# Optimization experiments

Hardware: AMD Instinct MI355X
Metric: run time of the kernel (lower is better)

The kernel has to match this reference:

```python
import jax, jax.numpy as jnp
import numpy as np

B, S, NX, H = 8, 1024, 1024, 16
HD = NX // H  # head dim = 64
MASKED_BIAS = -10000.0


def setup_inputs() -> dict:
    key = jax.random.key(0)
    ks = jax.random.split(key, 6)
    return {
        "x": jax.random.normal(ks[0], (B, S, NX), dtype=jnp.float32),
        "query": jax.random.normal(ks[1], (B, S, NX), dtype=jnp.float32),
        "c_attn_w": jax.random.normal(ks[2], (NX, 3 * NX), dtype=jnp.float32) * 0.02,
        "c_attn_b": jnp.zeros((3 * NX,), dtype=jnp.float32),
        "c_proj_w": jax.random.normal(ks[3], (NX, NX), dtype=jnp.float32) * 0.02,
        "c_proj_b": jnp.zeros((NX,), dtype=jnp.float32),
    }


def _split_heads(t):
    # [B, S, NX] -> [B, H, S, HD]
    b, s, _ = t.shape
    return t.reshape(b, s, H, HD).transpose(0, 2, 1, 3)


def reference(x, query, c_attn_w, c_attn_b, c_proj_w, c_proj_b):
    # Conv1D: y = x @ W + b
    kv = x @ c_attn_w + c_attn_b          # [B,S,3NX]; use key/value slices
    qy = query @ c_attn_w + c_attn_b      # [B,S,3NX]; use query slice
    q = _split_heads(qy[..., :NX])                     # [B,H,S,HD]
    k = _split_heads(kv[..., NX:2 * NX])               # [B,H,S,HD]
    v = _split_heads(kv[..., 2 * NX:])                 # [B,H,S,HD]

    w = jnp.einsum("bhqd,bhkd->bhqk", q, k) / jnp.sqrt(jnp.float32(HD))
    causal = jnp.tril(jnp.ones((S, S), dtype=bool))[None, None]
    w = jnp.where(causal, w, jnp.float32(MASKED_BIAS))
    w = jax.nn.softmax(w, axis=-1)
    a = jnp.einsum("bhqk,bhkd->bhqd", w, v)            # [B,H,S,HD]
    a = a.transpose(0, 2, 1, 3).reshape(B, S, NX)      # merge heads
    return a @ c_proj_w + c_proj_b
```

## Files before the change

### kernel.cpp

```cpp
#include <hip/hip_runtime.h>
#include <cstdint>
#include <cstddef>

#define Bb   8
#define Ss   1024
#define NXx  1024
#define Hh   16
#define HDd  64
#define Mm   (Bb*Ss)

typedef __bf16 bf16x8 __attribute__((ext_vector_type(8)));
typedef float  f32x4  __attribute__((ext_vector_type(4)));

__device__ __forceinline__ unsigned short f2bf(float f) {
    union { float f; unsigned int u; } v; v.f = f;
    return (unsigned short)((v.u + 0x8000u) >> 16);
}

__device__ __forceinline__ void load_lds16(const unsigned short* g, unsigned short* lds_base) {
    __builtin_amdgcn_global_load_lds(
        (const __attribute__((address_space(1))) void*)g,
        (__attribute__((address_space(3))) void*)lds_base, 16, 0, 0);
}

__global__ __launch_bounds__(256) void prep(
    const float* __restrict__ x, const float* __restrict__ query,
    const float* __restrict__ caw, const float* __restrict__ cpw,
    unsigned short* __restrict__ xb, unsigned short* __restrict__ qb,
    unsigned short* __restrict__ Wt, unsigned short* __restrict__ Pt)
{
    __shared__ float tile[32][33];
    const int bid = blockIdx.x;
    const int tid = threadIdx.x;

    if (bid < 16384) {
        const float* in = (bid < 8192) ? x : query;
        unsigned short* out = (bid < 8192) ? xb : qb;
        const int i = ((bid & 8191) * 256 + tid) * 4;
        const float4 v = *(const float4*)(in + i);
        unsigned long long p = (unsigned long long)f2bf(v.x)
            | ((unsigned long long)f2bf(v.y) << 16)
            | ((unsigned long long)f2bf(v.z) << 32)
            | ((unsigned long long)f2bf(v.w) << 48);
        *(unsigned long long*)(out + i) = p;
        return;
    }

    const float* in;
    unsigned short* out;
    int C, t;
    if (bid < 16384 + 3072) { in = caw; out = Wt; C = 3072; t = bid - 16384; }
    else                    { in = cpw; out = Pt; C = 1024; t = bid - 19456; }
    const int ntx = C >> 5;
    const int c0 = (t % ntx) * 32, r0 = (t / ntx) * 32;
    const int tx = tid & 31, ty = tid >> 5;
    for (int i = ty; i < 32; i += 8)
        tile[i][tx] = in[(size_t)(r0 + i) * C + c0 + tx];
    __syncthreads();
    for (int i = ty; i < 32; i += 8)
        out[(size_t)(c0 + i) * 1024 + r0 + tx] = f2bf(tile[tx][i]);
}

__global__ __launch_bounds__(256) void gemm128(
    const unsigned short* __restrict__ Ax,
    const unsigned short* __restrict__ Aq,
    const unsigned short* __restrict__ Bt,
    const float* __restrict__ bias,
    int K, int mode,
    unsigned short* __restrict__ out_q,
    unsigned short* __restrict__ out_k,
    unsigned short* __restrict__ out_v,
    float* __restrict__ out_f)
{
    __shared__ unsigned short smem[16384];
    unsigned short (*As)[64] = (unsigned short (*)[64])(smem);
    unsigned short (*Bs)[64] = (unsigned short (*)[64])(smem + 8192);

    const int tid  = threadIdx.x;
    const int w    = tid >> 6;
    const int lane = tid & 63;

    const int nx   = (mode == 0) ? 24 : 8;
    const int nxh  = nx >> 1;
    const int n    = blockIdx.x;
    const int xcd  = n & 7;
    const int sgrp = n >> 3;
    const int m0   = ((xcd >> 1) * 16 + sgrp / nxh) * 128;
    const int n0   = ((xcd & 1) * nxh + sgrp % nxh) * 128;
    const int region = n0 >> 10;
    const unsigned short* A = (mode == 0 && region == 0) ? Aq : Ax;

    const int wm   = (w >> 1) * 64;
    const int wn   = (w & 1) * 64;
    const int lrow = lane & 15;
    const int quad = lane >> 4;

    f32x4 acc[4][4] = {};

    const int rr   = lane >> 3;
    const int scol = (((lane & 7) ^ ((lane >> 4) & 3)) << 3);
    const unsigned short* Ag = A  + (size_t)(m0 + w * 32 + rr) * K + scol;
    const unsigned short* Bg = Bt + (size_t)(n0 + w * 32 + rr) * K + scol;
    unsigned short* ldsA = smem + (w * 32) * 64;
    unsigned short* ldsB = smem + 8192 + (w * 32) * 64;

    const int sw = (lrow >> 1) & 3;

    for (int k0 = 0; k0 < K; k0 += 64) {
        __syncthreads();
#pragma unroll
        for (int c = 0; c < 4; ++c) {
            load_lds16(Ag + (size_t)(c * 8) * K + k0, ldsA + c * 512);
            load_lds16(Bg + (size_t)(c * 8) * K + k0, ldsB + c * 512);
        }
        __syncthreads();
#pragma unroll
        for (int kk = 0; kk < 2; ++kk) {
            bf16x8 af[4], bfr[4];
            const int pc = (((kk * 4 + quad) ^ sw) << 3);
#pragma unroll
            for (int i = 0; i < 4; ++i) {
                af[i]  = *(const bf16x8*)&As[wm + i * 16 + lrow][pc];
                bfr[i] = *(const bf16x8*)&Bs[wn + i * 16 + lrow][pc];
            }
#pragma unroll
            for (int i = 0; i < 4; ++i)
#pragma unroll
                for (int j = 0; j < 4; ++j)
                    acc[i][j] = __builtin_amdgcn_mfma_f32_16x16x32_bf16(af[i], bfr[j], acc[i][j], 0, 0, 0);
        }
    }

    __syncthreads();

    if (mode == 1) {
#pragma unroll
        for (int i = 0; i < 4; ++i)
#pragma unroll
            for (int j = 0; j < 4; ++j) {
                const int ncol = n0 + wn + j * 16 + lrow;
                const float bv = bias[ncol];
#pragma unroll
                for (int r = 0; r < 4; ++r) {
                    const int mrow = m0 + wm + i * 16 + quad * 4 + r;
                    out_f[(size_t)mrow * NXx + ncol] = acc[i][j][r] + bv;
                }
            }
        return;
    }

    unsigned short* ep = smem + w * 2048;

    if (region != 2) {
        unsigned short* outp = (region == 0) ? out_q : out_k;
#pragma unroll
        for (int j = 0; j < 4; ++j) {
            const float bv = bias[n0 + wn + j * 16 + lrow];
#pragma unroll
            for (int i = 0; i < 4; ++i)
#pragma unroll
                for (int r = 0; r < 4; ++r)
                    ep[(i * 16 + quad * 4 + r) * 24 + lrow] = f2bf(acc[i][j][r] + bv);
#pragma unroll
            for (int t = 0; t < 2; ++t) {
                const int c    = t * 64 + lane;
                const int row  = c >> 1, ch = (c & 1) * 8;
                const int mrow = m0 + wm + row;
                const int cc   = (n0 + wn + j * 16 + ch) & (NXx - 1);
                const int hh   = cc >> 6, dd = cc & 63;
                const int bh   = (mrow >> 10) * Hh + hh;
                const int ss   = mrow & (Ss - 1);
                *(uint4*)&outp[((size_t)bh * Ss + ss) * HDd + dd] =
                    *(const uint4*)&ep[row * 24 + ch];
            }
        }
    } else {
#pragma unroll
        for (int j = 0; j < 4; ++j) {
            const float bv = bias[n0 + wn + j * 16 + lrow];
#pragma unroll
            for (int i = 0; i < 4; ++i)
#pragma unroll
                for (int r = 0; r < 4; ++r)
                    ep[lrow * 72 + i * 16 + quad * 4 + r] = f2bf(acc[i][j][r] + bv);
#pragma unroll
            for (int t = 0; t < 2; ++t) {
                const int c    = t * 64 + lane;
                const int col  = c >> 3, rc = (c & 7) * 8;
                const int cc   = (n0 + wn + j * 16 + col) & (NXx - 1);
                const int hh   = cc >> 6, dd = cc & 63;
                const int mrow = m0 + wm + rc;
                const int bh   = (mrow >> 10) * Hh + hh;
                const int ss   = mrow & (Ss - 1);
                *(uint4*)&out_v[((size_t)bh * HDd + dd) * Ss + ss] =
                    *(const uint4*)&ep[col * 72 + rc];
            }
        }
    }
}

__global__ __launch_bounds__(256) void flash_attn(
    const unsigned short* __restrict__ Qh,
    const unsigned short* __restrict__ Kh,
    const unsigned short* __restrict__ Vt,
    unsigned short* __restrict__ about)
{
    __shared__ unsigned short Ks[64][64];
    __shared__ unsigned short Vs[64][64];
    __shared__ unsigned short Pl[4][16][72];

    const int tid  = threadIdx.x;
    const int w    = tid >> 6;
    const int lane = tid & 63;
    const int bh   = blockIdx.x & 127;
    const int pr   = blockIdx.x >> 7;
    const int b    = bh >> 4, h = bh & 15;
    const int lrow = lane & 15;
    const int quad = lane >> 4;

    const unsigned short* Qb = Qh + (size_t)bh * Ss * HDd;
    const unsigned short* Kb = Kh + (size_t)bh * Ss * HDd;
    const unsigned short* Vb = Vt + (size_t)bh * HDd * Ss;

    const int sr = lane >> 3;
    const int lc = (((lane & 7) ^ ((lane >> 4) & 3)) << 3);
    unsigned short* ldsK0 = &Ks[w * 16][0];
    unsigned short* ldsK1 = &Ks[w * 16 + 8][0];
    unsigned short* ldsV0 = &Vs[w * 16][0];
    unsigned short* ldsV1 = &Vs[w * 16 + 8][0];

    const int sw = (lrow >> 1) & 3;
    const int ca = ((quad ^ sw) << 3);
    const int cb = (((4 + quad) ^ sw) << 3);

    for (int half = 0; half < 2; ++half) {
        const int qt    = half ? (15 - pr) : pr;
        const int qBase = qt * 64 + w * 16;

        const bf16x8 aq0 = *(const bf16x8*)(Qb + (size_t)(qBase + lrow) * HDd + quad * 8);
        const bf16x8 aq1 = *(const bf16x8*)(Qb + (size_t)(qBase + lrow) * HDd + 32 + quad * 8);

        f32x4 O[4] = {};
        float lsum[4] = { 0.f, 0.f, 0.f, 0.f };

        const int nkt = qt + 1;
        for (int kt = 0; kt < nkt; ++kt) {
            const int k0 = kt * 64;

            __syncthreads();
            load_lds16(Kb + (size_t)(k0 + w * 16 + sr) * HDd + lc,     ldsK0);
            load_lds16(Kb + (size_t)(k0 + w * 16 + sr + 8) * HDd + lc, ldsK1);
            load_lds16(Vb + (size_t)(w * 16 + sr) * Ss + k0 + lc,      ldsV0);
            load_lds16(Vb + (size_t)(w * 16 + sr + 8) * Ss + k0 + lc,  ldsV1);
            __syncthreads();

            f32x4 s[4] = {};
#pragma unroll
            for (int j = 0; j < 4; ++j) {
                bf16x8 b0 = *(const bf16x8*)&Ks[j * 16 + lrow][ca];
                bf16x8 b1 = *(const bf16x8*)&Ks[j * 16 + lrow][cb];
                s[j] = __builtin_amdgcn_mfma_f32_16x16x32_bf16(aq0, b0, s[j], 0, 0, 0);
                s[j] = __builtin_amdgcn_mfma_f32_16x16x32_bf16(aq1, b1, s[j], 0, 0, 0);
            }

            const bool diag = (kt == qt);
#pragma unroll
            for (int r = 0; r < 4; ++r) {
                const int q = qBase + quad * 4 + r;
#pragma unroll
                for (int j = 0; j < 4; ++j) {
                    float e = __expf(s[j][r] * 0.125f);
                    if (diag && (k0 + j * 16 + lrow > q)) e = 0.f;
                    lsum[r] += e;
                    Pl[w][quad * 4 + r][j * 16 + lrow] = f2bf(e);
                }
            }

            const bf16x8 ap0 = *(const bf16x8*)&Pl[w][lrow][quad * 8];
            const bf16x8 ap1 = *(const bf16x8*)&Pl[w][lrow][32 + quad * 8];
#pragma unroll
            for (int f = 0; f < 4; ++f) {
                bf16x8 bv0 = *(const bf16x8*)&Vs[f * 16 + lrow][ca];
                bf16x8 bv1 = *(const bf16x8*)&Vs[f * 16 + lrow][cb];
                O[f] = __builtin_amdgcn_mfma_f32_16x16x32_bf16(ap0, bv0, O[f], 0, 0, 0);
                O[f] = __builtin_amdgcn_mfma_f32_16x16x32_bf16(ap1, bv1, O[f], 0, 0, 0);
            }
        }

#pragma unroll
        for (int r = 0; r < 4; ++r) {
            float l = lsum[r];
            l += __shfl_xor(l, 1);
            l += __shfl_xor(l, 2);
            l += __shfl_xor(l, 4);
            l += __shfl_xor(l, 8);
            const float inv = 1.0f / l;
            const int q = qBase + quad * 4 + r;
            const size_t base = ((size_t)b * Ss + q) * NXx + h * HDd;
#pragma unroll
            for (int f = 0; f < 4; ++f)
                about[base + f * 16 + lrow] = f2bf(O[f][r] * inv);
        }
    }
}

extern "C" void kernel_launch(void* const* d_in, const int* in_sizes, int n_in,
                              void* d_out, int out_size, void* d_ws, size_t ws_size,
                              hipStream_t stream) {
    const float* x        = (const float*)d_in[0];
    const float* query    = (const float*)d_in[1];
    const float* c_attn_w = (const float*)d_in[2];
    const float* c_attn_b = (const float*)d_in[3];
    const float* c_proj_w = (const float*)d_in[4];
    const float* c_proj_b = (const float*)d_in[5];
    float* out = (float*)d_out;

    const size_t nTok = (size_t)Mm * NXx;
    char* ws = (char*)d_ws;
    unsigned short* xb    = (unsigned short*)ws;                 ws += nTok * 2;
    unsigned short* qb    = (unsigned short*)ws;                 ws += nTok * 2;
    unsigned short* Wt    = (unsigned short*)ws;                 ws += (size_t)3 * NXx * NXx * 2;
    unsigned short* Pt    = (unsigned short*)ws;                 ws += (size_t)NXx * NXx * 2;
    unsigned short* Qh    = (unsigned short*)ws;                 ws += nTok * 2;
    unsigned short* Kh    = (unsigned short*)ws;                 ws += nTok * 2;
    unsigned short* Vt    = (unsigned short*)ws;                 ws += nTok * 2;
    unsigned short* about = (unsigned short*)ws;                 ws += nTok * 2;
    if ((size_t)(ws - (char*)d_ws) > ws_size) return;

    prep<<<20480, 256, 0, stream>>>(x, query, c_attn_w, c_proj_w, xb, qb, Wt, Pt);

    gemm128<<<dim3(24 * 64), 256, 0, stream>>>(xb, qb, Wt, c_attn_b, NXx, 0,
                                               Qh, Kh, Vt, nullptr);
    flash_attn<<<1024, 256, 0, stream>>>(Qh, Kh, Vt, about);

    gemm128<<<dim3(8 * 64), 256, 0, stream>>>(about, nullptr, Pt, c_proj_b, NXx, 1,
                                              nullptr, nullptr, nullptr, out);
}
```

Before: 264.9 us.

## Enlarge flash-attention query tile to 128 rows and widen LDS XOR swizzle

The attention kernel now gives each block 128 query rows, 32 per wave in two 16-row groups, so every K/V tile loaded into LDS feeds twice as many MFMAs. This halves the grid and the total K/V traffic. Waves whose rows lie entirely above a key tile skip its compute but still join the barriers. The LDS XOR swizzle in both the GEMM and attention kernels changes from a 2-bit to a 3-bit pattern over the row index, meant to cut bank conflicts on the 16-byte fragment reads. In exchange the kernel uses more registers, has fewer blocks for load balance, and has some wave idle time on causal tiles.

```diff
diff --git a/kernel.cpp b/kernel.cpp
--- a/kernel.cpp
+++ b/kernel.cpp
@@ -98,13 +98,13 @@
     f32x4 acc[4][4] = {};
 
     const int rr   = lane >> 3;
-    const int scol = (((lane & 7) ^ ((lane >> 4) & 3)) << 3);
+    const int scol = (((lane & 7) ^ (lane >> 3)) << 3);
     const unsigned short* Ag = A  + (size_t)(m0 + w * 32 + rr) * K + scol;
     const unsigned short* Bg = Bt + (size_t)(n0 + w * 32 + rr) * K + scol;
     unsigned short* ldsA = smem + (w * 32) * 64;
     unsigned short* ldsB = smem + 8192 + (w * 32) * 64;
 
-    const int sw = (lrow >> 1) & 3;
+    const int swz = lrow & 7;
 
     for (int k0 = 0; k0 < K; k0 += 64) {
         __syncthreads();
@@ -117,7 +117,7 @@
 #pragma unroll
         for (int kk = 0; kk < 2; ++kk) {
             bf16x8 af[4], bfr[4];
-            const int pc = (((kk * 4 + quad) ^ sw) << 3);
+            const int pc = (((kk * 4 + quad) ^ swz) << 3);
 #pragma unroll
             for (int i = 0; i < 4; ++i) {
                 af[i]  = *(const bf16x8*)&As[wm + i * 16 + lrow][pc];
@@ -207,7 +207,7 @@
 {
     __shared__ unsigned short Ks[64][64];
     __shared__ unsigned short Vs[64][64];
-    __shared__ unsigned short Pl[4][16][72];
+    __shared__ unsigned short Pl[4][32][72];
 
     const int tid  = threadIdx.x;
     const int w    = tid >> 6;
@@ -223,27 +223,31 @@
     const unsigned short* Vb = Vt + (size_t)bh * HDd * Ss;
 
     const int sr = lane >> 3;
-    const int lc = (((lane & 7) ^ ((lane >> 4) & 3)) << 3);
+    const int lc = (((lane & 7) ^ (lane >> 3)) << 3);
     unsigned short* ldsK0 = &Ks[w * 16][0];
     unsigned short* ldsK1 = &Ks[w * 16 + 8][0];
     unsigned short* ldsV0 = &Vs[w * 16][0];
     unsigned short* ldsV1 = &Vs[w * 16 + 8][0];
 
-    const int sw = (lrow >> 1) & 3;
-    const int ca = ((quad ^ sw) << 3);
-    const int cb = (((4 + quad) ^ sw) << 3);
+    const int swz = lrow & 7;
+    const int ca = ((quad ^ swz) << 3);
+    const int cb = (((4 + quad) ^ swz) << 3);
 
     for (int half = 0; half < 2; ++half) {
-        const int qt    = half ? (15 - pr) : pr;
-        const int qBase = qt * 64 + w * 16;
-
-        const bf16x8 aq0 = *(const bf16x8*)(Qb + (size_t)(qBase + lrow) * HDd + quad * 8);
-        const bf16x8 aq1 = *(const bf16x8*)(Qb + (size_t)(qBase + lrow) * HDd + 32 + quad * 8);
-
-        f32x4 O[4] = {};
-        float lsum[4] = { 0.f, 0.f, 0.f, 0.f };
-
-        const int nkt = qt + 1;
+        const int qt = half ? (7 - pr) : pr;
+        const int qw = qt * 128 + w * 32;
+
+        bf16x8 aq[2][2];
+#pragma unroll
+        for (int g = 0; g < 2; ++g)
+#pragma unroll
+            for (int c = 0; c < 2; ++c)
+                aq[g][c] = *(const bf16x8*)(Qb + (size_t)(qw + g * 16 + lrow) * HDd + c * 32 + quad * 8);
+
+        f32x4 O[2][4] = {};
+        float lsum[2][4] = {};
+
+        const int nkt = 2 * qt + 2;
         for (int kt = 0; kt < nkt; ++kt) {
             const int k0 = kt * 64;
 
@@ -254,53 +258,67 @@
             load_lds16(Vb + (size_t)(w * 16 + sr + 8) * Ss + k0 + lc,  ldsV1);
             __syncthreads();
 
-            f32x4 s[4] = {};
+            if (k0 > qw + 31) continue;
+
+            f32x4 s[2][4] = {};
 #pragma unroll
             for (int j = 0; j < 4; ++j) {
-                bf16x8 b0 = *(const bf16x8*)&Ks[j * 16 + lrow][ca];
-                bf16x8 b1 = *(const bf16x8*)&Ks[j * 16 + lrow][cb];
-                s[j] = __builtin_amdgcn_mfma_f32_16x16x32_bf16(aq0, b0, s[j], 0, 0, 0);
-                s[j] = __builtin_amdgcn_mfma_f32_16x16x32_bf16(aq1, b1, s[j], 0, 0, 0);
-            }
-
-            const bool diag = (kt == qt);
+                const bf16x8 b0 = *(const bf16x8*)&Ks[j * 16 + lrow][ca];
+                const bf16x8 b1 = *(const bf16x8*)&Ks[j * 16 + lrow][cb];
+                s[0][j] = __builtin_amdgcn_mfma_f32_16x16x32_bf16(aq[0][0], b0, s[0][j], 0, 0, 0);
+                s[0][j] = __builtin_amdgcn_mfma_f32_16x16x32_bf16(aq[0][1], b1, s[0][j], 0, 0, 0);
+                s[1][j] = __builtin_amdgcn_mfma_f32_16x16x32_bf16(aq[1][0], b0, s[1][j], 0, 0, 0);
+                s[1][j] = __builtin_amdgcn_mfma_f32_16x16x32_bf16(aq[1][1], b1, s[1][j], 0, 0, 0);
+            }
+
+            const bool needMask = (k0 + 63 > qw);
+#pragma unroll
+            for (int g = 0; g < 2; ++g)
+#pragma unroll
+                for (int r = 0; r < 4; ++r) {
+                    const int q = qw + g * 16 + quad * 4 + r;
+#pragma unroll
+                    for (int j = 0; j < 4; ++j) {
+                        float e = __expf(s[g][j][r] * 0.125f);
+                        if (needMask && (k0 + j * 16 + lrow > q)) e = 0.f;
+                        lsum[g][r] += e;
+                        Pl[w][g * 16 + quad * 4 + r][j * 16 + lrow] = f2bf(e);
+                    }
+                }
+
+            bf16x8 ap[2][2];
+#pragma unroll
+            for (int g = 0; g < 2; ++g)
+#pragma unroll
+                for (int c = 0; c < 2; ++c)
+                    ap[g][c] = *(const bf16x8*)&Pl[w][g * 16 + lrow][c * 32 + quad * 8];
+#pragma unroll
+            for (int f = 0; f < 4; ++f) {
+                const bf16x8 bv0 = *(const bf16x8*)&Vs[f * 16 + lrow][ca];
+                const bf16x8 bv1 = *(const bf16x8*)&Vs[f * 16 + lrow][cb];
+                O[0][f] = __builtin_amdgcn_mfma_f32_16x16x32_bf16(ap[0][0], bv0, O[0][f], 0, 0, 0);
+                O[0][f] = __builtin_amdgcn_mfma_f32_16x16x32_bf16(ap[0][1], bv1, O[0][f], 0, 0, 0);
+                O[1][f] = __builtin_amdgcn_mfma_f32_16x16x32_bf16(ap[1][0], bv0, O[1][f], 0, 0, 0);
+                O[1][f] = __builtin_amdgcn_mfma_f32_16x16x32_bf16(ap[1][1], bv1, O[1][f], 0, 0, 0);
+            }
+        }
+
+#pragma unroll
+        for (int g = 0; g < 2; ++g)
 #pragma unroll
             for (int r = 0; r < 4; ++r) {
-                const int q = qBase + quad * 4 + r;
-#pragma unroll
-                for (int j = 0; j < 4; ++j) {
-                    float e = __expf(s[j][r] * 0.125f);
-                    if (diag && (k0 + j * 16 + lrow > q)) e = 0.f;
-                    lsum[r] += e;
-                    Pl[w][quad * 4 + r][j * 16 + lrow] = f2bf(e);
-                }
-            }
-
-            const bf16x8 ap0 = *(const bf16x8*)&Pl[w][lrow][quad * 8];
-            const bf16x8 ap1 = *(const bf16x8*)&Pl[w][lrow][32 + quad * 8];
-#pragma unroll
-            for (int f = 0; f < 4; ++f) {
-                bf16x8 bv0 = *(const bf16x8*)&Vs[f * 16 + lrow][ca];
-                bf16x8 bv1 = *(const bf16x8*)&Vs[f * 16 + lrow][cb];
-                O[f] = __builtin_amdgcn_mfma_f32_16x16x32_bf16(ap0, bv0, O[f], 0, 0, 0);
-                O[f] = __builtin_amdgcn_mfma_f32_16x16x32_bf16(ap1, bv1, O[f], 0, 0, 0);
-            }
-        }
-
-#pragma unroll
-        for (int r = 0; r < 4; ++r) {
-            float l = lsum[r];
-            l += __shfl_xor(l, 1);
-            l += __shfl_xor(l, 2);
-            l += __shfl_xor(l, 4);
-            l += __shfl_xor(l, 8);
-            const float inv = 1.0f / l;
-            const int q = qBase + quad * 4 + r;
-            const size_t base = ((size_t)b * Ss + q) * NXx + h * HDd;
-#pragma unroll
-            for (int f = 0; f < 4; ++f)
-                about[base + f * 16 + lrow] = f2bf(O[f][r] * inv);
-        }
+                float l = lsum[g][r];
+                l += __shfl_xor(l, 1);
+                l += __shfl_xor(l, 2);
+                l += __shfl_xor(l, 4);
+                l += __shfl_xor(l, 8);
+                const float inv = 1.0f / l;
+                const int q = qw + g * 16 + quad * 4 + r;
+                const size_t base = ((size_t)b * Ss + q) * NXx + h * HDd;
+#pragma unroll
+                for (int f = 0; f < 4; ++f)
+                    about[base + f * 16 + lrow] = f2bf(O[g][f][r] * inv);
+            }
     }
 }
 
@@ -331,7 +349,7 @@
 
     gemm128<<<dim3(24 * 64), 256, 0, stream>>>(xb, qb, Wt, c_attn_b, NXx, 0,
                                                Qh, Kh, Vt, nullptr);
-    flash_attn<<<1024, 256, 0, stream>>>(Qh, Kh, Vt, about);
+    flash_attn<<<512, 256, 0, stream>>>(Qh, Kh, Vt, about);
 
     gemm128<<<dim3(8 * 64), 256, 0, stream>>>(about, nullptr, Pt, c_proj_b, NXx, 1,
                                               nullptr, nullptr, nullptr, out);
```

New measurement: 266.2 us. No clear change (+0.5%).
